# Optimization experiments

Measured on AMD Instinct MI355X. Metric: run time of the kernel, lower is better.

The kernel has to match this reference:

```python
import jax, jax.numpy as jnp
import numpy as np

N_NODES = 40000
N_EDGES = 640000
D_IN = 512
D_OUT = 128


def setup_inputs() -> dict:
    key = jax.random.key(0)
    k_x, k_w, k_a, k_v, k_r, k_c = jax.random.split(key, 6)
    # Xavier-uniform bound for Linear(in=512, out=128)
    bound = float(np.sqrt(6.0 / (D_IN + D_OUT)))
    x = jax.random.normal(k_x, (N_NODES, D_IN), dtype=jnp.float32)
    weight = jax.random.uniform(k_w, (D_OUT, D_IN), dtype=jnp.float32,
                                minval=-bound, maxval=bound)
    bias = jnp.zeros((D_OUT,), dtype=jnp.float32)
    # PReLU default init is 0.25 (single shared slope)
    alpha = jnp.full((1,), 0.25, dtype=jnp.float32)
    edge_val = jax.random.uniform(k_v, (N_EDGES,), dtype=jnp.float32)
    edge_row = jax.random.randint(k_r, (N_EDGES,), 0, N_NODES, dtype=jnp.int32)
    edge_col = jax.random.randint(k_c, (N_EDGES,), 0, N_NODES, dtype=jnp.int32)
    return {"x": x, "weight": weight, "bias": bias, "alpha": alpha,
            "edge_val": edge_val, "edge_row": edge_row, "edge_col": edge_col}


def reference(x, weight, bias, alpha, edge_val, edge_row, edge_col):
    # seq = fc_1(input): [N, D_out]
    seq = jnp.einsum('ni,oi->no', x, weight)
    # torch.spmm(adj, seq) with adj in COO form:
    # out[r] = sum over edges (r, c, v) of v * seq[c]
    msgs = edge_val[:, None] * seq[edge_col]          # [E, D_out]
    agg = jax.ops.segment_sum(msgs, edge_row, num_segments=x.shape[0])
    agg = agg + bias
    # PReLU with a single shared slope alpha
    return jnp.where(agg > 0, agg, alpha[0] * agg)
```

## Files before the change

### kernel.cpp

```cpp
#include <hip/hip_runtime.h>
#include <hip/hip_bf16.h>

#define N_NODES 40000
#define N_EDGES 640000
#define D_IN 512
#define D_OUT 128
#define BM 128
#define BK 64
#define CAP 128
#define NB_GE 313
#define EPT 4
#define NB_SC 625

typedef __attribute__((ext_vector_type(4))) float f32x4;
typedef __attribute__((ext_vector_type(8))) short bf16x8;
typedef __attribute__((ext_vector_type(4))) unsigned short us4;

static __device__ __forceinline__ unsigned short f2bf(float f) {
    unsigned int u = __float_as_uint(f);
    unsigned int r = u + 0x7fffu + ((u >> 16) & 1u);
    return (unsigned short)(r >> 16);
}

__global__ void zero_kernel(int* __restrict__ p, int n) {
    int i = blockIdx.x * blockDim.x + threadIdx.x;
    if (i < n) p[i] = 0;
}

__global__ __launch_bounds__(256) void fused_kernel(
    const float* __restrict__ x, const float* __restrict__ w,
    unsigned short* __restrict__ seq,
    const int* __restrict__ erow, const int* __restrict__ ecol,
    const float* __restrict__ eval, int* __restrict__ cursor,
    float2* __restrict__ bucket)
{
    if (blockIdx.x >= NB_GE) {
        const int base = (blockIdx.x - NB_GE) * (256 * EPT) + threadIdx.x;
        int r[EPT], c[EPT];
        float v[EPT];
        #pragma unroll
        for (int k = 0; k < EPT; k++) {
            int e = base + k * 256;
            r[k] = erow[e]; c[k] = ecol[e]; v[k] = eval[e];
        }
        int slot[EPT];
        #pragma unroll
        for (int k = 0; k < EPT; k++) slot[k] = atomicAdd(&cursor[r[k]], 1);
        #pragma unroll
        for (int k = 0; k < EPT; k++)
            bucket[(size_t)r[k] * CAP + slot[k]] = make_float2(v[k], __int_as_float(c[k]));
        return;
    }

    __shared__ unsigned short As[BM * BK];
    __shared__ unsigned short Bs[D_OUT * BK];

    const int tid = threadIdx.x;
    const int lane = tid & 63;
    const int wv = tid >> 6;
    const int block_row = blockIdx.x * BM;
    const int srow = tid >> 3;
    const int scol = (tid & 7) * 8;

    f32x4 ra[4][2], rb[4][2];

    auto issue_loads = [&](int k0) {
        #pragma unroll
        for (int p = 0; p < 4; ++p) {
            int gr = block_row + srow + p * 32; if (gr >= N_NODES) gr = N_NODES - 1;
            const float* sa = x + (size_t)gr * D_IN + k0 + scol;
            ra[p][0] = *(const f32x4*)sa;
            ra[p][1] = *(const f32x4*)(sa + 4);
            const float* sb = w + (size_t)(srow + p * 32) * D_IN + k0 + scol;
            rb[p][0] = *(const f32x4*)sb;
            rb[p][1] = *(const f32x4*)(sb + 4);
        }
    };

    f32x4 acc[2][8];
    #pragma unroll
    for (int i = 0; i < 2; i++)
        #pragma unroll
        for (int j = 0; j < 8; j++)
            acc[i][j] = f32x4{0.f, 0.f, 0.f, 0.f};

    issue_loads(0);

    for (int kt = 0; kt < D_IN / BK; ++kt) {
        __syncthreads();
        #pragma unroll
        for (int p = 0; p < 4; ++p) {
            int r = srow + p * 32;
            us4 h0, h1, g0, g1;
            #pragma unroll
            for (int q = 0; q < 4; q++) {
                h0[q] = f2bf(ra[p][0][q]); h1[q] = f2bf(ra[p][1][q]);
                g0[q] = f2bf(rb[p][0][q]); g1[q] = f2bf(rb[p][1][q]);
            }
            int off = (r * (BK * 2) + scol * 2) ^ ((r & 7) << 4);
            *(us4*)((char*)As + off)     = h0;
            *(us4*)((char*)As + off + 8) = h1;
            *(us4*)((char*)Bs + off)     = g0;
            *(us4*)((char*)Bs + off + 8) = g1;
        }
        if (kt < D_IN / BK - 1) issue_loads((kt + 1) * BK);
        __syncthreads();

        #pragma unroll
        for (int ks = 0; ks < 2; ++ks) {
            const int kb = ks * 32 + (lane >> 4) * 8;
            bf16x8 a[2], b[8];
            #pragma unroll
            for (int m = 0; m < 2; m++) {
                int r = wv * 32 + m * 16 + (lane & 15);
                int off = (r * (BK * 2) + kb * 2) ^ ((r & 7) << 4);
                a[m] = *(const bf16x8*)((const char*)As + off);
            }
            #pragma unroll
            for (int n = 0; n < 8; n++) {
                int r = n * 16 + (lane & 15);
                int off = (r * (BK * 2) + kb * 2) ^ ((r & 7) << 4);
                b[n] = *(const bf16x8*)((const char*)Bs + off);
            }
            #pragma unroll
            for (int m = 0; m < 2; m++)
                #pragma unroll
                for (int n = 0; n < 8; n++)
                    acc[m][n] = __builtin_amdgcn_mfma_f32_16x16x32_bf16(a[m], b[n], acc[m][n], 0, 0, 0);
        }
    }

    #pragma unroll
    for (int m = 0; m < 2; m++) {
        #pragma unroll
        for (int r = 0; r < 4; r++) {
            int grow = block_row + wv * 32 + m * 16 + (lane >> 4) * 4 + r;
            if (grow < N_NODES) {
                #pragma unroll
                for (int n = 0; n < 8; n++) {
                    int col = n * 16 + (lane & 15);
                    seq[(size_t)grow * D_OUT + col] = f2bf(acc[m][n][r]);
                }
            }
        }
    }
}

__global__ __launch_bounds__(256) void agg_kernel(
    const unsigned short* __restrict__ seq, const int* __restrict__ cursor,
    const float2* __restrict__ bucket, const float* __restrict__ bias,
    const float* __restrict__ alpha, float* __restrict__ out)
{
    const int row = blockIdx.x * 4 + (threadIdx.x >> 6);
    const int lane = threadIdx.x & 63;
    const int cnt = cursor[row];
    const float2* b = bucket + (size_t)row * CAP;

    float a0 = 0.f, a1 = 0.f;
    int e = 0;
    for (; e + 4 <= cnt; e += 4) {
        float2 q0 = b[e], q1 = b[e + 1], q2 = b[e + 2], q3 = b[e + 3];
        unsigned int p0 = *(const unsigned int*)(seq + (size_t)__float_as_uint(q0.y) * D_OUT + lane * 2);
        unsigned int p1 = *(const unsigned int*)(seq + (size_t)__float_as_uint(q1.y) * D_OUT + lane * 2);
        unsigned int p2 = *(const unsigned int*)(seq + (size_t)__float_as_uint(q2.y) * D_OUT + lane * 2);
        unsigned int p3 = *(const unsigned int*)(seq + (size_t)__float_as_uint(q3.y) * D_OUT + lane * 2);
        a0 += q0.x * __uint_as_float(p0 << 16);
        a1 += q0.x * __uint_as_float(p0 & 0xffff0000u);
        a0 += q1.x * __uint_as_float(p1 << 16);
        a1 += q1.x * __uint_as_float(p1 & 0xffff0000u);
        a0 += q2.x * __uint_as_float(p2 << 16);
        a1 += q2.x * __uint_as_float(p2 & 0xffff0000u);
        a0 += q3.x * __uint_as_float(p3 << 16);
        a1 += q3.x * __uint_as_float(p3 & 0xffff0000u);
    }
    for (; e < cnt; ++e) {
        float2 q0 = b[e];
        unsigned int p0 = *(const unsigned int*)(seq + (size_t)__float_as_uint(q0.y) * D_OUT + lane * 2);
        a0 += q0.x * __uint_as_float(p0 << 16);
        a1 += q0.x * __uint_as_float(p0 & 0xffff0000u);
    }
    float al = alpha[0];
    float2 bi = *(const float2*)(bias + lane * 2);
    float r0 = a0 + bi.x;
    float r1 = a1 + bi.y;
    r0 = r0 > 0.f ? r0 : al * r0;
    r1 = r1 > 0.f ? r1 : al * r1;
    *(float2*)(out + (size_t)row * D_OUT + lane * 2) = make_float2(r0, r1);
}

extern "C" void kernel_launch(void* const* d_in, const int* in_sizes, int n_in,
                              void* d_out, int out_size, void* d_ws, size_t ws_size,
                              hipStream_t stream)
{
    (void)in_sizes; (void)n_in; (void)out_size; (void)ws_size;
    const float* x     = (const float*)d_in[0];
    const float* w     = (const float*)d_in[1];
    const float* bias  = (const float*)d_in[2];
    const float* alpha = (const float*)d_in[3];
    const float* eval  = (const float*)d_in[4];
    const int*   erow  = (const int*)d_in[5];
    const int*   ecol  = (const int*)d_in[6];
    float* out = (float*)d_out;

    char* ws = (char*)d_ws;
    unsigned short* seq = (unsigned short*)ws;
    int*    cursor = (int*)(ws + 10240000);
    float2* bucket = (float2*)(ws + 10400000);

    zero_kernel<<<(N_NODES + 255) / 256, 256, 0, stream>>>(cursor, N_NODES);
    fused_kernel<<<NB_GE + NB_SC, 256, 0, stream>>>(x, w, seq, erow, ecol, eval, cursor, bucket);
    agg_kernel<<<N_NODES / 4, 256, 0, stream>>>(seq, cursor, bucket, bias, alpha, out);
}
```

Before: 194.2 us.

## Prepack bf16 weights, drop LDS GEMM, and shard edge buckets per XCD

Adds a prep kernel that converts the weight matrix to bf16 once in MFMA fragment order and zeroes eight per-XCD cursor arrays. The GEMM becomes one wave per 32-row tile that reads A straight from global memory with a two-deep register prefetch and reads B fragments from the prepacked buffer, so there is no LDS staging and no __syncthreads. The bucketing phase now indexes its cursor and bucket copy by hardware XCD id to spread atomics across dies, uses 8 edges per thread, and is launched before the GEMM blocks. In exchange, aggregation must scan eight sub-buckets per row, and a per-copy capacity of 48 risks overflow for high-degree rows.

```diff
diff --git a/kernel.cpp b/kernel.cpp
--- a/kernel.cpp
+++ b/kernel.cpp
@@ -5,12 +5,12 @@
 #define N_EDGES 640000
 #define D_IN 512
 #define D_OUT 128
-#define BM 128
-#define BK 64
-#define CAP 128
+#define NCOPY 8
+#define CAPC 48
+#define NB_SC 313
+#define EPT 8
 #define NB_GE 313
-#define EPT 4
-#define NB_SC 625
+#define N_TILES 1250
 
 typedef __attribute__((ext_vector_type(4))) float f32x4;
 typedef __attribute__((ext_vector_type(8))) short bf16x8;
@@ -22,125 +22,129 @@
     return (unsigned short)(r >> 16);
 }
 
-__global__ void zero_kernel(int* __restrict__ p, int n) {
-    int i = blockIdx.x * blockDim.x + threadIdx.x;
-    if (i < n) p[i] = 0;
+__global__ __launch_bounds__(256) void prep_kernel(
+    const float* __restrict__ w, unsigned short* __restrict__ pb,
+    int* __restrict__ cursor)
+{
+    if (blockIdx.x < 32) {
+        int e = blockIdx.x * 256 + threadIdx.x;
+        int l = e & 63, n = (e >> 6) & 7, k = e >> 9;
+        int o = n * 16 + (l & 15);
+        int kk = k * 32 + ((l >> 4) << 3);
+        const float* src = w + (size_t)o * D_IN + kk;
+        f32x4 v0 = *(const f32x4*)src;
+        f32x4 v1 = *(const f32x4*)(src + 4);
+        us4 h0, h1;
+        #pragma unroll
+        for (int q = 0; q < 4; q++) { h0[q] = f2bf(v0[q]); h1[q] = f2bf(v1[q]); }
+        *(us4*)(pb + e * 8)     = h0;
+        *(us4*)(pb + e * 8 + 4) = h1;
+    } else {
+        int i = (blockIdx.x - 32) * 256 + threadIdx.x;
+        if (i < NCOPY * N_NODES) cursor[i] = 0;
+    }
 }
 
 __global__ __launch_bounds__(256) void fused_kernel(
-    const float* __restrict__ x, const float* __restrict__ w,
+    const float* __restrict__ x, const unsigned short* __restrict__ pb,
     unsigned short* __restrict__ seq,
     const int* __restrict__ erow, const int* __restrict__ ecol,
     const float* __restrict__ eval, int* __restrict__ cursor,
     float2* __restrict__ bucket)
 {
-    if (blockIdx.x >= NB_GE) {
-        const int base = (blockIdx.x - NB_GE) * (256 * EPT) + threadIdx.x;
+    if (blockIdx.x < NB_SC) {
+        unsigned int xcd;
+        xcd = __builtin_amdgcn_s_getreg(20 | (0 << 6) | (7 << 11)) & 7;
+        int* cur = cursor + (size_t)xcd * N_NODES;
+        const int base = blockIdx.x * (256 * EPT) + threadIdx.x;
         int r[EPT], c[EPT];
         float v[EPT];
-        #pragma unroll
-        for (int k = 0; k < EPT; k++) {
-            int e = base + k * 256;
-            r[k] = erow[e]; c[k] = ecol[e]; v[k] = eval[e];
+        bool ok[EPT];
+        #pragma unroll
+        for (int j = 0; j < EPT; j++) {
+            int e = base + j * 256;
+            ok[j] = e < N_EDGES;
+            int es = ok[j] ? e : 0;
+            r[j] = erow[es]; c[j] = ecol[es]; v[j] = eval[es];
         }
         int slot[EPT];
         #pragma unroll
-        for (int k = 0; k < EPT; k++) slot[k] = atomicAdd(&cursor[r[k]], 1);
-        #pragma unroll
-        for (int k = 0; k < EPT; k++)
-            bucket[(size_t)r[k] * CAP + slot[k]] = make_float2(v[k], __int_as_float(c[k]));
+        for (int j = 0; j < EPT; j++)
+            if (ok[j]) slot[j] = atomicAdd(&cur[r[j]], 1);
+        #pragma unroll
+        for (int j = 0; j < EPT; j++)
+            if (ok[j])
+                bucket[((size_t)r[j] * NCOPY + xcd) * CAPC + slot[j]] =
+                    make_float2(v[j], __int_as_float(c[j]));
         return;
     }
 
-    __shared__ unsigned short As[BM * BK];
-    __shared__ unsigned short Bs[D_OUT * BK];
-
-    const int tid = threadIdx.x;
-    const int lane = tid & 63;
-    const int wv = tid >> 6;
-    const int block_row = blockIdx.x * BM;
-    const int srow = tid >> 3;
-    const int scol = (tid & 7) * 8;
-
-    f32x4 ra[4][2], rb[4][2];
-
-    auto issue_loads = [&](int k0) {
-        #pragma unroll
-        for (int p = 0; p < 4; ++p) {
-            int gr = block_row + srow + p * 32; if (gr >= N_NODES) gr = N_NODES - 1;
-            const float* sa = x + (size_t)gr * D_IN + k0 + scol;
-            ra[p][0] = *(const f32x4*)sa;
-            ra[p][1] = *(const f32x4*)(sa + 4);
-            const float* sb = w + (size_t)(srow + p * 32) * D_IN + k0 + scol;
-            rb[p][0] = *(const f32x4*)sb;
-            rb[p][1] = *(const f32x4*)(sb + 4);
-        }
-    };
+    const int lane = threadIdx.x & 63;
+    const int wv = threadIdx.x >> 6;
+    const int tile = (blockIdx.x - NB_SC) * 4 + wv;
+    if (tile >= N_TILES) return;
+    const int r0 = tile * 32;
+    const int arow = lane & 15;
+    const int koff = (lane >> 4) << 3;
 
     f32x4 acc[2][8];
     #pragma unroll
-    for (int i = 0; i < 2; i++)
-        #pragma unroll
-        for (int j = 0; j < 8; j++)
-            acc[i][j] = f32x4{0.f, 0.f, 0.f, 0.f};
-
-    issue_loads(0);
-
-    for (int kt = 0; kt < D_IN / BK; ++kt) {
-        __syncthreads();
-        #pragma unroll
-        for (int p = 0; p < 4; ++p) {
-            int r = srow + p * 32;
-            us4 h0, h1, g0, g1;
+    for (int m = 0; m < 2; m++)
+        #pragma unroll
+        for (int n = 0; n < 8; n++)
+            acc[m][n] = f32x4{0.f, 0.f, 0.f, 0.f};
+
+    f32x4 af[2][2][2];
+    const float* xa0 = x + (size_t)(r0 + arow) * D_IN + koff;
+    const float* xa1 = x + (size_t)(r0 + 16 + arow) * D_IN + koff;
+
+    #define LOAD_A(buf, k)  do {                                  \
+        af[buf][0][0] = *(const f32x4*)(xa0 + (k) * 32);          \
+        af[buf][0][1] = *(const f32x4*)(xa0 + (k) * 32 + 4);      \
+        af[buf][1][0] = *(const f32x4*)(xa1 + (k) * 32);          \
+        af[buf][1][1] = *(const f32x4*)(xa1 + (k) * 32 + 4);      \
+    } while (0)
+
+    LOAD_A(0, 0);
+    LOAD_A(1, 1);
+
+    #pragma unroll
+    for (int k = 0; k < 16; k++) {
+        const int cur = k & 1;
+        bf16x8 a[2];
+        #pragma unroll
+        for (int m = 0; m < 2; m++) {
+            us4 h0, h1;
             #pragma unroll
             for (int q = 0; q < 4; q++) {
-                h0[q] = f2bf(ra[p][0][q]); h1[q] = f2bf(ra[p][1][q]);
-                g0[q] = f2bf(rb[p][0][q]); g1[q] = f2bf(rb[p][1][q]);
+                h0[q] = f2bf(af[cur][m][0][q]);
+                h1[q] = f2bf(af[cur][m][1][q]);
             }
-            int off = (r * (BK * 2) + scol * 2) ^ ((r & 7) << 4);
-            *(us4*)((char*)As + off)     = h0;
-            *(us4*)((char*)As + off + 8) = h1;
-            *(us4*)((char*)Bs + off)     = g0;
-            *(us4*)((char*)Bs + off + 8) = g1;
-        }
-        if (kt < D_IN / BK - 1) issue_loads((kt + 1) * BK);
-        __syncthreads();
-
-        #pragma unroll
-        for (int ks = 0; ks < 2; ++ks) {
-            const int kb = ks * 32 + (lane >> 4) * 8;
-            bf16x8 a[2], b[8];
+            a[m] = (bf16x8)(__attribute__((ext_vector_type(8))) unsigned short){
+                h0[0], h0[1], h0[2], h0[3], h1[0], h1[1], h1[2], h1[3]};
+        }
+        if (k < 14) LOAD_A(cur, k + 2);
+        bf16x8 b[8];
+        #pragma unroll
+        for (int n = 0; n < 8; n++)
+            b[n] = *(const bf16x8*)(pb + (((k * 8 + n) * 64 + lane) << 3));
+        #pragma unroll
+        for (int n = 0; n < 8; n++)
             #pragma unroll
-            for (int m = 0; m < 2; m++) {
-                int r = wv * 32 + m * 16 + (lane & 15);
-                int off = (r * (BK * 2) + kb * 2) ^ ((r & 7) << 4);
-                a[m] = *(const bf16x8*)((const char*)As + off);
-            }
+            for (int m = 0; m < 2; m++)
+                acc[m][n] = __builtin_amdgcn_mfma_f32_16x16x32_bf16(a[m], b[n], acc[m][n], 0, 0, 0);
+    }
+    #undef LOAD_A
+
+    #pragma unroll
+    for (int m = 0; m < 2; m++) {
+        #pragma unroll
+        for (int r = 0; r < 4; r++) {
+            int grow = r0 + m * 16 + (lane >> 4) * 4 + r;
             #pragma unroll
             for (int n = 0; n < 8; n++) {
-                int r = n * 16 + (lane & 15);
-                int off = (r * (BK * 2) + kb * 2) ^ ((r & 7) << 4);
-                b[n] = *(const bf16x8*)((const char*)Bs + off);
-            }
-            #pragma unroll
-            for (int m = 0; m < 2; m++)
-                #pragma unroll
-                for (int n = 0; n < 8; n++)
-                    acc[m][n] = __builtin_amdgcn_mfma_f32_16x16x32_bf16(a[m], b[n], acc[m][n], 0, 0, 0);
-        }
-    }
-
-    #pragma unroll
-    for (int m = 0; m < 2; m++) {
-        #pragma unroll
-        for (int r = 0; r < 4; r++) {
-            int grow = block_row + wv * 32 + m * 16 + (lane >> 4) * 4 + r;
-            if (grow < N_NODES) {
-                #pragma unroll
-                for (int n = 0; n < 8; n++) {
-                    int col = n * 16 + (lane & 15);
-                    seq[(size_t)grow * D_OUT + col] = f2bf(acc[m][n][r]);
-                }
+                int col = n * 16 + (lane & 15);
+                seq[(size_t)grow * D_OUT + col] = f2bf(acc[m][n][r]);
             }
         }
     }
@@ -153,31 +157,34 @@
 {
     const int row = blockIdx.x * 4 + (threadIdx.x >> 6);
     const int lane = threadIdx.x & 63;
-    const int cnt = cursor[row];
-    const float2* b = bucket + (size_t)row * CAP;
 
     float a0 = 0.f, a1 = 0.f;
-    int e = 0;
-    for (; e + 4 <= cnt; e += 4) {
-        float2 q0 = b[e], q1 = b[e + 1], q2 = b[e + 2], q3 = b[e + 3];
-        unsigned int p0 = *(const unsigned int*)(seq + (size_t)__float_as_uint(q0.y) * D_OUT + lane * 2);
-        unsigned int p1 = *(const unsigned int*)(seq + (size_t)__float_as_uint(q1.y) * D_OUT + lane * 2);
-        unsigned int p2 = *(const unsigned int*)(seq + (size_t)__float_as_uint(q2.y) * D_OUT + lane * 2);
-        unsigned int p3 = *(const unsigned int*)(seq + (size_t)__float_as_uint(q3.y) * D_OUT + lane * 2);
-        a0 += q0.x * __uint_as_float(p0 << 16);
-        a1 += q0.x * __uint_as_float(p0 & 0xffff0000u);
-        a0 += q1.x * __uint_as_float(p1 << 16);
-        a1 += q1.x * __uint_as_float(p1 & 0xffff0000u);
-        a0 += q2.x * __uint_as_float(p2 << 16);
-        a1 += q2.x * __uint_as_float(p2 & 0xffff0000u);
-        a0 += q3.x * __uint_as_float(p3 << 16);
-        a1 += q3.x * __uint_as_float(p3 & 0xffff0000u);
-    }
-    for (; e < cnt; ++e) {
-        float2 q0 = b[e];
-        unsigned int p0 = *(const unsigned int*)(seq + (size_t)__float_as_uint(q0.y) * D_OUT + lane * 2);
-        a0 += q0.x * __uint_as_float(p0 << 16);
-        a1 += q0.x * __uint_as_float(p0 & 0xffff0000u);
+    #pragma unroll
+    for (int c = 0; c < NCOPY; c++) {
+        const int cnt = cursor[(size_t)c * N_NODES + row];
+        const float2* b = bucket + ((size_t)row * NCOPY + c) * CAPC;
+        int e = 0;
+        for (; e + 4 <= cnt; e += 4) {
+            float2 q0 = b[e], q1 = b[e + 1], q2 = b[e + 2], q3 = b[e + 3];
+            unsigned int p0 = *(const unsigned int*)(seq + (size_t)__float_as_uint(q0.y) * D_OUT + lane * 2);
+            unsigned int p1 = *(const unsigned int*)(seq + (size_t)__float_as_uint(q1.y) * D_OUT + lane * 2);
+            unsigned int p2 = *(const unsigned int*)(seq + (size_t)__float_as_uint(q2.y) * D_OUT + lane * 2);
+            unsigned int p3 = *(const unsigned int*)(seq + (size_t)__float_as_uint(q3.y) * D_OUT + lane * 2);
+            a0 += q0.x * __uint_as_float(p0 << 16);
+            a1 += q0.x * __uint_as_float(p0 & 0xffff0000u);
+            a0 += q1.x * __uint_as_float(p1 << 16);
+            a1 += q1.x * __uint_as_float(p1 & 0xffff0000u);
+            a0 += q2.x * __uint_as_float(p2 << 16);
+            a1 += q2.x * __uint_as_float(p2 & 0xffff0000u);
+            a0 += q3.x * __uint_as_float(p3 << 16);
+            a1 += q3.x * __uint_as_float(p3 & 0xffff0000u);
+        }
+        for (; e < cnt; ++e) {
+            float2 q0 = b[e];
+            unsigned int p0 = *(const unsigned int*)(seq + (size_t)__float_as_uint(q0.y) * D_OUT + lane * 2);
+            a0 += q0.x * __uint_as_float(p0 << 16);
+            a1 += q0.x * __uint_as_float(p0 & 0xffff0000u);
+        }
     }
     float al = alpha[0];
     float2 bi = *(const float2*)(bias + lane * 2);
@@ -205,9 +212,10 @@
     char* ws = (char*)d_ws;
     unsigned short* seq = (unsigned short*)ws;
     int*    cursor = (int*)(ws + 10240000);
-    float2* bucket = (float2*)(ws + 10400000);
-
-    zero_kernel<<<(N_NODES + 255) / 256, 256, 0, stream>>>(cursor, N_NODES);
-    fused_kernel<<<NB_GE + NB_SC, 256, 0, stream>>>(x, w, seq, erow, ecol, eval, cursor, bucket);
+    unsigned short* pb = (unsigned short*)(ws + 11520000);
+    float2* bucket = (float2*)(ws + 11651072);
+
+    prep_kernel<<<1282, 256, 0, stream>>>(w, pb, cursor);
+    fused_kernel<<<NB_SC + NB_GE, 256, 0, stream>>>(x, pb, seq, erow, ecol, eval, cursor, bucket);
     agg_kernel<<<N_NODES / 4, 256, 0, stream>>>(seq, cursor, bucket, bias, alpha, out);
 }
```

Result: slower. 282.2 us (+45.3%).
